# Performance work log

Measured on AMD Instinct MI355X. Metric: run time of the kernel, lower is better.

## Reference

```python
import jax, jax.numpy as jnp
import numpy as np

B, S, D, H, F = 2, 1024, 2048, 16, 8192
DH = D // H
MAX_ALPHA = 0.2
CN_SCALE = D / (D - 1)  # CenterNorm scale factor dim/(dim-1)


def setup_inputs() -> dict:
    key = jax.random.key(0)
    ks = jax.random.split(key, 8)
    s = 0.02
    f32 = jnp.float32
    return {
        "x": jax.random.normal(ks[0], (B, S, D), f32),
        "ln1_g": jnp.ones((D,), f32), "ln1_b": jnp.zeros((D,), f32),
        "wq": jax.random.normal(ks[1], (D, D), f32) * s, "bq": jnp.zeros((D,), f32),
        "wk": jax.random.normal(ks[2], (D, D), f32) * s, "bk": jnp.zeros((D,), f32),
        "wv": jax.random.normal(ks[3], (D, D), f32) * s, "bv": jnp.zeros((D,), f32),
        "wo": jax.random.normal(ks[4], (D, D), f32) * s, "bo": jnp.zeros((D,), f32),
        "tau": jnp.ones((H,), f32),   # learnable per-head temperature, init_tau=1.0
        "nu": jnp.ones((H,), f32),    # learnable per-head output scale, init_nu=1.0
        "alpha1": jnp.full((D,), 0.1, f32),  # per-channel residual weight, init 0.1
        "ln2_g": jnp.ones((D,), f32), "ln2_b": jnp.zeros((D,), f32),
        "w1": jax.random.normal(ks[5], (F, D), f32) * s, "b1": jnp.zeros((F,), f32),
        "w2": jax.random.normal(ks[6], (D, F), f32) * s, "b2": jnp.zeros((D,), f32),
        "alpha2": jnp.full((D,), 0.1, f32),
    }


def _center_norm(x, g, b):
    # CenterNorm: subtract mean only (no variance), scale by dim/(dim-1)
    mu = jnp.mean(x, axis=-1, keepdims=True)
    return g * (CN_SCALE * (x - mu)) + b


def _l2norm(t):
    return t / (jnp.linalg.norm(t, axis=-1, keepdims=True) + 1e-6)


def _cosine_attn(x, wq, bq, wk, bk, wv, bv, wo, bo, tau, nu):
    # project and split heads -> [B,H,S,DH]
    def proj(w, b):
        return (jnp.einsum('bsd,ed->bse', x, w) + b).reshape(B, S, H, DH).transpose(0, 2, 1, 3)
    q, k, v = proj(wq, bq), proj(wk, bk), proj(wv, bv)
    qn, kn = _l2norm(q), _l2norm(k)  # cosine similarity attention
    scores = jnp.einsum('bhqd,bhkd->bhqk', qn, kn) * tau[None, :, None, None]
    causal = jnp.tril(jnp.ones((S, S), bool))
    scores = jnp.where(causal[None, None], scores, -jnp.inf)
    p = jax.nn.softmax(scores, axis=-1)
    o = jnp.einsum('bhqk,bhkd->bhqd', p, v) * nu[None, :, None, None]
    o = o.transpose(0, 2, 1, 3).reshape(B, S, D)
    return jnp.einsum('bsd,ed->bse', o, wo) + bo


def _ffn(x, w1, b1, w2, b2):
    h = jax.nn.gelu(jnp.einsum('bsd,fd->bsf', x, w1) + b1)
    return jnp.einsum('bsf,df->bsd', h, w2) + b2


def reference(x, ln1_g, ln1_b, wq, bq, wk, bk, wv, bv, wo, bo, tau, nu,
              alpha1, ln2_g, ln2_b, w1, b1, w2, b2, alpha2):
    a = _center_norm(x, ln1_g, ln1_b)
    a1 = jnp.clip(alpha1, -MAX_ALPHA, MAX_ALPHA)
    x1 = a + a1 * _cosine_attn(a, wq, bq, wk, bk, wv, bv, wo, bo, tau, nu)
    m = _center_norm(x1, ln2_g, ln2_b)
    a2 = jnp.clip(alpha2, -MAX_ALPHA, MAX_ALPHA)
    return m + a2 * _ffn(m, w1, b1, w2, b2)
```

## Files before the change

### kernel.cpp

```cpp
#include <hip/hip_runtime.h>
#include <hip/hip_bf16.h>
#include <stdint.h>

#define B_ 2
#define S_ 1024
#define D_ 2048
#define H_ 16
#define F_ 8192
#define DH_ 128
#define M_ 2048

typedef unsigned short u16;
typedef __attribute__((ext_vector_type(8))) short short8;
typedef __attribute__((ext_vector_type(4))) float f32x4;
typedef __attribute__((ext_vector_type(2))) float f32x2;

__device__ __forceinline__ u16 f2bf(float f) {
  union { float f; uint32_t u; } c; c.f = f;
  uint32_t r = c.u + 0x7FFFu + ((c.u >> 16) & 1u);
  return (u16)(r >> 16);
}

__device__ __forceinline__ float bf2f(u16 v) {
  union { uint32_t u; float f; } c; c.u = ((uint32_t)v) << 16;
  return c.f;
}

__device__ __forceinline__ void gload16(const void* g, void* l) {
  __builtin_amdgcn_global_load_lds((const __attribute__((address_space(1))) void*)g,
                                   (__attribute__((address_space(3))) void*)l, 16, 0, 0);
}

__device__ __forceinline__ float clipa(float a) {
  return fminf(0.2f, fmaxf(-0.2f, a));
}

__device__ __forceinline__ float gelu_f(float x) {
  float z = 0.7978845608028654f * (x + 0.044715f * x * x * x);
  z = fminf(10.f, fmaxf(-10.f, z));
  float e = __expf(2.f * z);
  return 0.5f * x * (1.f + (e - 1.f) / (e + 1.f));
}

__global__ __launch_bounds__(256) void k_cvt_half(const float* __restrict__ wq,
                                                  const float* __restrict__ wk,
                                                  const float* __restrict__ wv,
                                                  const float* __restrict__ wo,
                                                  const float* __restrict__ w1,
                                                  const float* __restrict__ w2,
                                                  u16* __restrict__ dst, int base) {
  const int gi = base + blockIdx.x * 256 + threadIdx.x;
  const float* s;
  int off;
  if (gi < 2097152) {
    int r = gi >> 19;
    s = r == 0 ? wq : (r == 1 ? wk : (r == 2 ? wv : wo));
    off = gi & 524287;
  } else if (gi < 4194304) {
    s = w1; off = gi - 2097152;
  } else {
    s = w2; off = gi - 4194304;
  }
  f32x4 a = *(const f32x4*)(s + (size_t)off * 8);
  f32x4 b = *(const f32x4*)(s + (size_t)off * 8 + 4);
  short8 o;
  o[0] = (short)f2bf(a[0]); o[1] = (short)f2bf(a[1]);
  o[2] = (short)f2bf(a[2]); o[3] = (short)f2bf(a[3]);
  o[4] = (short)f2bf(b[0]); o[5] = (short)f2bf(b[1]);
  o[6] = (short)f2bf(b[2]); o[7] = (short)f2bf(b[3]);
  *(short8*)(dst + (size_t)gi * 8) = o;
}

__global__ __launch_bounds__(256) void k_centernorm(const float* __restrict__ x,
                                                    const float* __restrict__ g,
                                                    const float* __restrict__ bb,
                                                    float* __restrict__ of,
                                                    u16* __restrict__ ob) {
  const int row = blockIdx.x;
  const int t = threadIdx.x;
  const float* xr = x + (size_t)row * D_;
  f32x4 v0 = *(const f32x4*)(xr + t * 8);
  f32x4 v1 = *(const f32x4*)(xr + t * 8 + 4);
  float s = v0[0] + v0[1] + v0[2] + v0[3] + v1[0] + v1[1] + v1[2] + v1[3];
#pragma unroll
  for (int off = 1; off < 64; off <<= 1) s += __shfl_xor(s, off);
  __shared__ float red[4];
  if ((t & 63) == 0) red[t >> 6] = s;
  __syncthreads();
  const float mu = (red[0] + red[1] + red[2] + red[3]) * (1.0f / D_);
  const float CNS = (float)D_ / (float)(D_ - 1);
  f32x4 g0 = *(const f32x4*)(g + t * 8);
  f32x4 g1 = *(const f32x4*)(g + t * 8 + 4);
  f32x4 b0 = *(const f32x4*)(bb + t * 8);
  f32x4 b1 = *(const f32x4*)(bb + t * 8 + 4);
  f32x4 y0, y1;
  short8 yb;
#pragma unroll
  for (int i = 0; i < 4; i++) {
    y0[i] = g0[i] * (CNS * (v0[i] - mu)) + b0[i];
    y1[i] = g1[i] * (CNS * (v1[i] - mu)) + b1[i];
  }
#pragma unroll
  for (int i = 0; i < 4; i++) { yb[i] = (short)f2bf(y0[i]); yb[4 + i] = (short)f2bf(y1[i]); }
  float* orow = of + (size_t)row * D_;
  *(f32x4*)(orow + t * 8) = y0;
  *(f32x4*)(orow + t * 8 + 4) = y1;
  *(short8*)(ob + (size_t)row * D_ + t * 8) = yb;
}

template <int EPI>
__device__ __forceinline__ void gemm256_core(const u16* __restrict__ A,
                                             const u16* __restrict__ Bt,
                                             const float* __restrict__ bias,
                                             float* __restrict__ outf,
                                             u16* __restrict__ outb,
                                             int N, int K, int kbase, int nk,
                                             int m0, int n0,
                                             const float* __restrict__ tau,
                                             u16* __restrict__ qkv, int z) {
  __shared__ char lds[2][65536];
  const int t = threadIdx.x;
  const int l = t & 63, w = t >> 6;
  const int wr = w >> 2, wc = w & 3;
  const int l15 = l & 15, lhi = l >> 4;
  const int sw = (l15 & 7) << 4;
  const int ab0 = l15 * 128 + ((lhi * 16) ^ sw);
  const int ab1 = l15 * 128 + ((64 + lhi * 16) ^ sw);

  auto stage = [&](int kt, int h) {
#pragma unroll
    for (int rj = 0; rj < 4; rj++) {
      const int region = rj >> 1, j = rj & 1;
      const int pl = h * 16384 + j * 8192 + t * 16;
      const int row = pl >> 7;
      const int scol = (pl & 127) ^ ((row & 7) << 4);
      const int grow = (region ? n0 : m0) + row;
      const char* src = (const char*)(region ? Bt : A) +
                        (size_t)grow * (size_t)(K * 2) +
                        (size_t)((kbase + kt * 64) * 2 + scol);
      gload16(src, &lds[kt & 1][region * 32768 + pl]);
    }
  };

  f32x4 acc[8][4] = {};

  stage(0, 0); stage(0, 1); stage(1, 0);
  asm volatile("s_waitcnt vmcnt(4)" ::: "memory");
  __builtin_amdgcn_s_barrier();
  __builtin_amdgcn_sched_barrier(0);

  for (int kt = 0; kt < nk; ++kt) {
    const char* base = &lds[kt & 1][0];
    const char* pA0 = base + wr * 4096 + ab0;
    const char* pA1 = base + wr * 4096 + ab1;
    const char* pB0 = base + 32768 + wc * 8192 + ab0;
    const char* pB1 = base + 32768 + wc * 8192 + ab1;
    short8 bf[4][2];
#pragma unroll
    for (int ni = 0; ni < 4; ni++) {
      bf[ni][0] = *(const short8*)(pB0 + ni * 2048);
      bf[ni][1] = *(const short8*)(pB1 + ni * 2048);
    }
#pragma unroll
    for (int q = 0; q < 4; q++) {
      short8 aq[2][2];
#pragma unroll
      for (int mi = 0; mi < 2; mi++) {
        aq[mi][0] = *(const short8*)(pA0 + q * 8192 + mi * 2048);
        aq[mi][1] = *(const short8*)(pA1 + q * 8192 + mi * 2048);
      }
      if (q == 1 && kt + 1 < nk) stage(kt + 1, 1);
      if (q == 3 && kt + 2 < nk) stage(kt + 2, 0);
      __builtin_amdgcn_s_setprio(1);
#pragma unroll
      for (int ks = 0; ks < 2; ks++)
#pragma unroll
        for (int mi = 0; mi < 2; mi++)
#pragma unroll
          for (int ni = 0; ni < 4; ni++)
            acc[q * 2 + mi][ni] = __builtin_amdgcn_mfma_f32_16x16x32_bf16(
                aq[mi][ks], bf[ni][ks], acc[q * 2 + mi][ni], 0, 0, 0);
      __builtin_amdgcn_s_setprio(0);
      if (q == 1) __builtin_amdgcn_s_barrier();
    }
    if (kt + 1 < nk) {
      if (kt + 2 < nk) { asm volatile("s_waitcnt vmcnt(4)" ::: "memory"); }
      else             { asm volatile("s_waitcnt vmcnt(0)" ::: "memory"); }
      __builtin_amdgcn_s_barrier();
      __builtin_amdgcn_sched_barrier(0);
    }
  }

  if constexpr (EPI == 4) {
    __shared__ float part[4][256];
#pragma unroll
    for (int ni = 0; ni < 4; ni++) {
      const float bc = bias[n0 + wc * 64 + ni * 16 + l15];
#pragma unroll
      for (int ai = 0; ai < 8; ai++)
#pragma unroll
        for (int j = 0; j < 4; j++) acc[ai][ni][j] += bc;
    }
    if (z < 2) {
      float p[8][4];
#pragma unroll
      for (int ai = 0; ai < 8; ai++)
#pragma unroll
        for (int j = 0; j < 4; j++) {
          p[ai][j] = acc[ai][0][j] * acc[ai][0][j] + acc[ai][1][j] * acc[ai][1][j] +
                     acc[ai][2][j] * acc[ai][2][j] + acc[ai][3][j] * acc[ai][3][j];
#pragma unroll
          for (int off = 1; off < 16; off <<= 1) p[ai][j] += __shfl_xor(p[ai][j], off);
        }
      if (l15 == 0) {
#pragma unroll
        for (int ai = 0; ai < 8; ai++)
#pragma unroll
          for (int j = 0; j < 4; j++) {
            const int rb = (ai >> 1) * 64 + wr * 32 + (ai & 1) * 16 + lhi * 4 + j;
            part[wc][rb] = p[ai][j];
          }
      }
    }
    __syncthreads();
    const int hl = wc >> 1;
    const int hglob = (n0 >> 7) + hl;
    const float tauh = (z == 0) ? tau[hglob] : 1.f;
    char* yt = (char*)&lds[0][0] + w * 16384;
#pragma unroll
    for (int ai = 0; ai < 8; ai++) {
#pragma unroll
      for (int j = 0; j < 4; j++) {
        float sc = 1.f;
        if (z < 2) {
          const int rb = (ai >> 1) * 64 + wr * 32 + (ai & 1) * 16 + lhi * 4 + j;
          const float ssq = part[2 * hl][rb] + part[2 * hl + 1][rb];
          sc = tauh / (sqrtf(ssq) + 1e-6f);
        }
        const int rl = (ai >> 1) * 32 + (ai & 1) * 16 + lhi * 4 + j;
        const int swz = (rl & 7) << 4;
#pragma unroll
        for (int ni = 0; ni < 4; ni++) {
          const int cbyte = (ni * 16 + l15) * 2;
          *(u16*)(yt + rl * 128 + (cbyte ^ swz)) = f2bf(acc[ai][ni][j] * sc);
        }
      }
    }
    __syncthreads();
#pragma unroll
    for (int pass = 0; pass < 16; pass++) {
      const int rl = pass * 8 + (l >> 3);
      const int cb = (l & 7) * 16;
      const short8 v = *(const short8*)(yt + rl * 128 + (cb ^ ((rl & 7) << 4)));
      const int m = m0 + ((rl >> 5) << 6) + wr * 32 + (rl & 31);
      const int bb2 = m >> 10, s = m & 1023;
      const int d = (wc & 1) * 64 + (cb >> 1);
      *(short8*)(qkv + (((size_t)(bb2 * H_ + hglob)) * S_ + s) * DH_ + d) = v;
    }
    return;
  }

#pragma unroll
  for (int ni = 0; ni < 4; ni++) {
    const int col = n0 + wc * 64 + ni * 16 + l15;
    const float bcol = (EPI == 3) ? 0.f : bias[col];
#pragma unroll
    for (int ai = 0; ai < 8; ai++) {
      const int row = m0 + (ai >> 1) * 64 + wr * 32 + (ai & 1) * 16 + lhi * 4;
#pragma unroll
      for (int j = 0; j < 4; j++) {
        const float v = acc[ai][ni][j] + bcol;
        const size_t idx = (size_t)(row + j) * N + col;
        if (EPI == 0) outf[idx] = v;
        else if (EPI == 2) outb[idx] = f2bf(gelu_f(v));
        else outb[idx] = f2bf(v);
      }
    }
  }
}

__global__ __launch_bounds__(512, 2) void k_qkv256(const u16* A, const u16* W,
                                                   const float* b0, const float* b1,
                                                   const float* b2, const float* tau,
                                                   u16* qn, u16* kn, u16* vn) {
  const int z = blockIdx.z;
  const u16* Bt = W + (size_t)z * 4194304;
  const float* bias = z == 0 ? b0 : (z == 1 ? b1 : b2);
  u16* dst = z == 0 ? qn : (z == 1 ? kn : vn);
  gemm256_core<4>(A, Bt, bias, nullptr, nullptr, D_, D_, 0, 32,
                  blockIdx.y * 256, blockIdx.x * 256, tau, dst, z);
}

__global__ __launch_bounds__(512, 2) void k_ffn1_256(const u16* A, const u16* Bt,
                                                     const float* bias, u16* outb) {
  gemm256_core<2>(A, Bt, bias, nullptr, outb, F_, D_, 0, 32,
                  blockIdx.y * 256, blockIdx.x * 256, nullptr, nullptr, 0);
}

__global__ __launch_bounds__(512, 2) void k_ffn2_256(const u16* A, const u16* Bt, u16* P) {
  gemm256_core<3>(A, Bt, nullptr, nullptr, P + (size_t)blockIdx.z * M_ * D_, D_, F_,
                  blockIdx.z * 2048, 32, blockIdx.y * 256, blockIdx.x * 256,
                  nullptr, nullptr, 0);
}

__global__ __launch_bounds__(256, 2) void k_oproj(const u16* __restrict__ A,
                                                  const u16* __restrict__ Bt,
                                                  const float* __restrict__ bias,
                                                  const float* __restrict__ res,
                                                  const float* __restrict__ alpha,
                                                  float* __restrict__ outf) {
  const int N = D_, K = D_, nk = 32;
  const int m0 = blockIdx.y * 128, n0 = blockIdx.x * 128;
  __shared__ char lds[2][32768];
  const int t = threadIdx.x;
  const int l = t & 63, w = t >> 6;
  const int wr = w >> 1, wc = w & 1;
  const int l15 = l & 15, lhi = l >> 4;
  const int sw = (l15 & 7) << 4;
  const int ab0 = l15 * 128 + ((lhi * 16) ^ sw);
  const int ab1 = l15 * 128 + ((64 + lhi * 16) ^ sw);

  auto stage = [&](int kt, int h) {
#pragma unroll
    for (int rj = 0; rj < 4; rj++) {
      const int region = rj >> 1, j = rj & 1;
      const int pl = h * 8192 + j * 4096 + t * 16;
      const int row = pl >> 7;
      const int scol = (pl & 127) ^ ((row & 7) << 4);
      const int grow = (region ? n0 : m0) + row;
      const char* src = (const char*)(region ? Bt : A) +
                        (size_t)grow * (size_t)(K * 2) + (size_t)(kt * 128 + scol);
      gload16(src, &lds[kt & 1][region * 16384 + pl]);
    }
  };

  f32x4 acc[4][4] = {};
  stage(0, 0); stage(0, 1); stage(1, 0);
  asm volatile("s_waitcnt vmcnt(4)" ::: "memory");
  __builtin_amdgcn_s_barrier();
  __builtin_amdgcn_sched_barrier(0);

  for (int kt = 0; kt < nk; ++kt) {
    const char* base = &lds[kt & 1][0];
    const char* pB0 = base + 16384 + wc * 8192 + ab0;
    const char* pB1 = base + 16384 + wc * 8192 + ab1;
    short8 bf[4][2];
#pragma unroll
    for (int ni = 0; ni < 4; ni++) {
      bf[ni][0] = *(const short8*)(pB0 + ni * 2048);
      bf[ni][1] = *(const short8*)(pB1 + ni * 2048);
    }
#pragma unroll
    for (int q = 0; q < 2; q++) {
      short8 aq[2][2];
#pragma unroll
      for (int mi = 0; mi < 2; mi++) {
        aq[mi][0] = *(const short8*)(base + q * 8192 + wr * 4096 + mi * 2048 + ab0);
        aq[mi][1] = *(const short8*)(base + q * 8192 + wr * 4096 + mi * 2048 + ab1);
      }
      if (q == 0 && kt + 1 < nk) stage(kt + 1, 1);
      if (q == 1 && kt + 2 < nk) stage(kt + 2, 0);
      __builtin_amdgcn_s_setprio(1);
#pragma unroll
      for (int ks = 0; ks < 2; ks++)
#pragma unroll
        for (int mi = 0; mi < 2; mi++)
#pragma unroll
          for (int ni = 0; ni < 4; ni++)
            acc[q * 2 + mi][ni] = __builtin_amdgcn_mfma_f32_16x16x32_bf16(
                aq[mi][ks], bf[ni][ks], acc[q * 2 + mi][ni], 0, 0, 0);
      __builtin_amdgcn_s_setprio(0);
      if (q == 0) __builtin_amdgcn_s_barrier();
    }
    if (kt + 1 < nk) {
      if (kt + 2 < nk) { asm volatile("s_waitcnt vmcnt(4)" ::: "memory"); }
      else             { asm volatile("s_waitcnt vmcnt(0)" ::: "memory"); }
      __builtin_amdgcn_s_barrier();
      __builtin_amdgcn_sched_barrier(0);
    }
  }

#pragma unroll
  for (int ni = 0; ni < 4; ni++) {
    const int col = n0 + wc * 64 + ni * 16 + l15;
    const float bcol = bias[col];
    const float alc = clipa(alpha[col]);
#pragma unroll
    for (int ai = 0; ai < 4; ai++) {
      const int row = m0 + (ai >> 1) * 64 + wr * 32 + (ai & 1) * 16 + lhi * 4;
#pragma unroll
      for (int j = 0; j < 4; j++) {
        const size_t idx = (size_t)(row + j) * N + col;
        outf[idx] = res[idx] + alc * (acc[ai][ni][j] + bcol);
      }
    }
  }
}

__global__ __launch_bounds__(256) void k_ffn2_combine(const u16* __restrict__ P,
                                                      const float* __restrict__ bias,
                                                      const float* __restrict__ res,
                                                      const float* __restrict__ alpha,
                                                      float* __restrict__ out) {
  const int i = blockIdx.x * 256 + threadIdx.x;
  const size_t base = (size_t)i * 8;
  const int col = (int)(base & (D_ - 1));
  const size_t PS = (size_t)M_ * D_;
  float s[8] = {};
#pragma unroll
  for (int p = 0; p < 4; p++) {
    short8 v = *(const short8*)(P + p * PS + base);
#pragma unroll
    for (int j = 0; j < 8; j++) s[j] += bf2f((u16)v[j]);
  }
  f32x4 b0 = *(const f32x4*)(bias + col);
  f32x4 b1 = *(const f32x4*)(bias + col + 4);
  f32x4 a0 = *(const f32x4*)(alpha + col);
  f32x4 a1 = *(const f32x4*)(alpha + col + 4);
  f32x4 r0 = *(const f32x4*)(res + base);
  f32x4 r1 = *(const f32x4*)(res + base + 4);
  f32x4 o0, o1;
#pragma unroll
  for (int j = 0; j < 4; j++) {
    o0[j] = r0[j] + clipa(a0[j]) * (s[j] + b0[j]);
    o1[j] = r1[j] + clipa(a1[j]) * (s[4 + j] + b1[j]);
  }
  *(f32x4*)(out + base) = o0;
  *(f32x4*)(out + base + 4) = o1;
}

__global__ __launch_bounds__(256) void k_attn(const u16* __restrict__ qn,
                                              const u16* __restrict__ kn,
                                              const u16* __restrict__ vn,
                                              const float* __restrict__ nu,
                                              u16* __restrict__ o) {
  __shared__ u16 Ks[64 * 128];
  __shared__ u16 Vt[128 * 64];
  __shared__ u16 Pl[4][16][72];
  const int t = threadIdx.x;
  const int l = t & 63, w = t >> 6;
  const int l15 = l & 15, lhi = l >> 4;
  const int qt = blockIdx.x;
  const int bh = blockIdx.y;
  const int h = bh & (H_ - 1);
  const int b = bh >> 4;
  const size_t hoff = (size_t)bh * S_ * DH_;
  const u16* Qh = qn + hoff;
  const u16* Kh = kn + hoff;
  const u16* Vh = vn + hoff;
  const int q0 = qt * 64;
  const int r0 = q0 + w * 16;
  short8 qf[4];
#pragma unroll
  for (int kk = 0; kk < 4; kk++)
    qf[kk] = *(const short8*)(Qh + (size_t)(r0 + l15) * DH_ + kk * 32 + lhi * 8);
  float mrow[4], lrow[4];
  f32x4 oacc[8] = {};
#pragma unroll
  for (int j = 0; j < 4; j++) { mrow[j] = -1e30f; lrow[j] = 0.f; }

  for (int kv0 = 0; kv0 < q0 + 64; kv0 += 64) {
#pragma unroll
    for (int i = 0; i < 4; i++) {
      const int p = i * 4096 + t * 16;
      const int row = p >> 8;
      const int colb = p & 255;
      const int scolb = colb ^ ((row & 7) << 4);
      gload16((const char*)(Kh + (size_t)(kv0 + row) * DH_) + scolb, (char*)Ks + p);
    }
#pragma unroll
    for (int i = 0; i < 4; i++) {
      const int c0 = w * 8 + i * 32;
      const int r = l;
      short8 vv = *(const short8*)(Vh + (size_t)(kv0 + r) * DH_ + c0);
#pragma unroll
      for (int j = 0; j < 8; j++) {
        const int ba = ((c0 + j) * 128 + r * 2) ^ (((c0 + j) & 7) << 4);
        *(u16*)((char*)Vt + ba) = (u16)vv[j];
      }
    }
    __syncthreads();
    f32x4 st[4] = {};
#pragma unroll
    for (int ks = 0; ks < 4; ks++) {
#pragma unroll
      for (int ct = 0; ct < 4; ct++) {
        const int n = ct * 16 + l15;
        const int ka = (ks * 32 + lhi * 8) * 2;
        short8 kf = *(const short8*)((const char*)Ks + n * 256 + (ka ^ ((n & 7) << 4)));
        st[ct] = __builtin_amdgcn_mfma_f32_16x16x32_bf16(qf[ks], kf, st[ct], 0, 0, 0);
      }
    }
    float pm[4] = {-1e30f, -1e30f, -1e30f, -1e30f};
#pragma unroll
    for (int ct = 0; ct < 4; ct++) {
      const int col = kv0 + ct * 16 + l15;
#pragma unroll
      for (int j = 0; j < 4; j++) {
        const int row = r0 + lhi * 4 + j;
        float s = st[ct][j];
        s = (col <= row) ? s : -1e30f;
        st[ct][j] = s;
        pm[j] = fmaxf(pm[j], s);
      }
    }
#pragma unroll
    for (int j = 0; j < 4; j++) {
#pragma unroll
      for (int off = 1; off < 16; off <<= 1) pm[j] = fmaxf(pm[j], __shfl_xor(pm[j], off));
    }
    float scl[4], psum[4];
#pragma unroll
    for (int j = 0; j < 4; j++) {
      const float nm = fmaxf(mrow[j], pm[j]);
      scl[j] = __expf(mrow[j] - nm);
      mrow[j] = nm;
      psum[j] = 0.f;
    }
#pragma unroll
    for (int ct = 0; ct < 4; ct++) {
#pragma unroll
      for (int j = 0; j < 4; j++) {
        const float p = __expf(st[ct][j] - mrow[j]);
        psum[j] += p;
        Pl[w][lhi * 4 + j][ct * 16 + l15] = f2bf(p);
      }
    }
#pragma unroll
    for (int j = 0; j < 4; j++) {
#pragma unroll
      for (int off = 1; off < 16; off <<= 1) psum[j] += __shfl_xor(psum[j], off);
      lrow[j] = lrow[j] * scl[j] + psum[j];
    }
#pragma unroll
    for (int nt = 0; nt < 8; nt++) {
#pragma unroll
      for (int j = 0; j < 4; j++) oacc[nt][j] *= scl[j];
    }
#pragma unroll
    for (int ks2 = 0; ks2 < 2; ks2++) {
      short8 pa = *(const short8*)((const char*)&Pl[w][0][0] + l15 * 144 + ks2 * 64 + lhi * 16);
#pragma unroll
      for (int nt = 0; nt < 8; nt++) {
        const int n = nt * 16 + l15;
        const int ba = (n * 128 + (ks2 * 32 + lhi * 8) * 2) ^ ((n & 7) << 4);
        short8 vf = *(const short8*)((const char*)Vt + ba);
        oacc[nt] = __builtin_amdgcn_mfma_f32_16x16x32_bf16(pa, vf, oacc[nt], 0, 0, 0);
      }
    }
    __syncthreads();
  }
  const float num = nu[h];
  float rs[4];
#pragma unroll
  for (int j = 0; j < 4; j++) rs[j] = num / lrow[j];
#pragma unroll
  for (int nt = 0; nt < 8; nt++) {
    const int col = h * DH_ + nt * 16 + l15;
#pragma unroll
    for (int j = 0; j < 4; j++) {
      const int row = r0 + lhi * 4 + j;
      o[((size_t)b * S_ + row) * D_ + col] = f2bf(oacc[nt][j] * rs[j]);
    }
  }
}

extern "C" void kernel_launch(void* const* d_in, const int* in_sizes, int n_in,
                              void* d_out, int out_size, void* d_ws, size_t ws_size,
                              hipStream_t stream) {
  const float* x    = (const float*)d_in[0];
  const float* ln1g = (const float*)d_in[1];
  const float* ln1b = (const float*)d_in[2];
  const float* wq   = (const float*)d_in[3];
  const float* bq   = (const float*)d_in[4];
  const float* wk   = (const float*)d_in[5];
  const float* bk   = (const float*)d_in[6];
  const float* wv   = (const float*)d_in[7];
  const float* bv   = (const float*)d_in[8];
  const float* wo   = (const float*)d_in[9];
  const float* bo   = (const float*)d_in[10];
  const float* tau  = (const float*)d_in[11];
  const float* nu   = (const float*)d_in[12];
  const float* al1  = (const float*)d_in[13];
  const float* ln2g = (const float*)d_in[14];
  const float* ln2b = (const float*)d_in[15];
  const float* w1   = (const float*)d_in[16];
  const float* b1   = (const float*)d_in[17];
  const float* w2   = (const float*)d_in[18];
  const float* b2   = (const float*)d_in[19];
  const float* al2  = (const float*)d_in[20];

  char* ws = (char*)d_ws;
  u16* WQ = (u16*)(ws + 0);
  u16* WO = (u16*)(ws + 25165824);
  u16* W1B = (u16*)(ws + 33554432);
  u16* W2B = (u16*)(ws + 67108864);
  float* AF = (float*)(ws + 100663296);
  u16*   AB = (u16*)(ws + 117440512);
  u16*   OB = (u16*)(ws + 125829120);
  u16*   MB = (u16*)(ws + 134217728);
  float* X1 = (float*)(ws + 142606336);
  float* MF2 = (float*)(ws + 159383552);
  u16* QN = (u16*)(ws + 176160768);
  u16* KN = (u16*)(ws + 184549376);
  u16* VN = (u16*)(ws + 192937984);
  u16*   HB = (u16*)(ws + 176160768);
  u16*   P4 = (u16*)(ws + 0);

  k_cvt_half<<<12288, 256, 0, stream>>>(wq, wk, wv, wo, w1, w2, WQ, 0);
  k_cvt_half<<<12288, 256, 0, stream>>>(wq, wk, wv, wo, w1, w2, WQ, 3145728);

  k_centernorm<<<M_, 256, 0, stream>>>(x, ln1g, ln1b, AF, AB);

  k_qkv256<<<dim3(8, 8, 3), 512, 0, stream>>>(AB, WQ, bq, bk, bv, tau, QN, KN, VN);

  k_attn<<<dim3(S_ / 64, B_ * H_), 256, 0, stream>>>(QN, KN, VN, nu, OB);

  k_oproj<<<dim3(16, 16), 256, 0, stream>>>(OB, WO, bo, AF, al1, X1);

  k_centernorm<<<M_, 256, 0, stream>>>(X1, ln2g, ln2b, MF2, MB);

  k_ffn1_256<<<dim3(32, 8), 512, 0, stream>>>(MB, W1B, b1, HB);

  k_ffn2_256<<<dim3(8, 8, 4), 512, 0, stream>>>(HB, W2B, P4);
  k_ffn2_combine<<<2048, 256, 0, stream>>>(P4, b2, MF2, al2, (float*)d_out);
}
```

Baseline: 372.5 us.

## Merge weight conversion into one kernel and rework GEMM staging pipeline

The two weight-conversion launches are replaced by one kernel in which each thread converts four 8-element chunks, with all loads issued before any conversion to raise memory-level parallelism. The 256-tile GEMM core now splits the next-tile global-to-LDS loads into four quarter-stages, one per inner q step, so B and A for the next k-tile are fetched in pieces across the compute of the current tile. Extra barriers and lgkmcnt waits are added every quarter step. That spreads memory traffic more evenly but adds synchronisation and reduces prefetch depth from two tiles to one.

```diff
diff --git a/kernel.cpp b/kernel.cpp
--- a/kernel.cpp
+++ b/kernel.cpp
@@ -42,33 +42,49 @@
   return 0.5f * x * (1.f + (e - 1.f) / (e + 1.f));
 }
 
-__global__ __launch_bounds__(256) void k_cvt_half(const float* __restrict__ wq,
-                                                  const float* __restrict__ wk,
-                                                  const float* __restrict__ wv,
-                                                  const float* __restrict__ wo,
-                                                  const float* __restrict__ w1,
-                                                  const float* __restrict__ w2,
-                                                  u16* __restrict__ dst, int base) {
-  const int gi = base + blockIdx.x * 256 + threadIdx.x;
-  const float* s;
-  int off;
-  if (gi < 2097152) {
-    int r = gi >> 19;
-    s = r == 0 ? wq : (r == 1 ? wk : (r == 2 ? wv : wo));
-    off = gi & 524287;
-  } else if (gi < 4194304) {
-    s = w1; off = gi - 2097152;
-  } else {
-    s = w2; off = gi - 4194304;
-  }
-  f32x4 a = *(const f32x4*)(s + (size_t)off * 8);
-  f32x4 b = *(const f32x4*)(s + (size_t)off * 8 + 4);
-  short8 o;
-  o[0] = (short)f2bf(a[0]); o[1] = (short)f2bf(a[1]);
-  o[2] = (short)f2bf(a[2]); o[3] = (short)f2bf(a[3]);
-  o[4] = (short)f2bf(b[0]); o[5] = (short)f2bf(b[1]);
-  o[6] = (short)f2bf(b[2]); o[7] = (short)f2bf(b[3]);
-  *(short8*)(dst + (size_t)gi * 8) = o;
+__global__ __launch_bounds__(256) void k_cvt_all(const float* __restrict__ wq,
+                                                 const float* __restrict__ wk,
+                                                 const float* __restrict__ wv,
+                                                 const float* __restrict__ wo,
+                                                 const float* __restrict__ w1,
+                                                 const float* __restrict__ w2,
+                                                 u16* __restrict__ dst) {
+  const int tid = blockIdx.x * 256 + threadIdx.x;
+  const float* s[4];
+  int gi[4];
+#pragma unroll
+  for (int k = 0; k < 4; k++) {
+    const int g = tid + k * 1572864;
+    gi[k] = g;
+    const float* p;
+    int off;
+    if (g < 2097152) {
+      const int r = g >> 19;
+      p = r == 0 ? wq : (r == 1 ? wk : (r == 2 ? wv : wo));
+      off = g & 524287;
+    } else if (g < 4194304) {
+      p = w1; off = g - 2097152;
+    } else {
+      p = w2; off = g - 4194304;
+    }
+    s[k] = p + (size_t)off * 8;
+  }
+  f32x4 a[4], b[4];
+#pragma unroll
+  for (int k = 0; k < 4; k++) {
+    a[k] = *(const f32x4*)(s[k]);
+    b[k] = *(const f32x4*)(s[k] + 4);
+  }
+  __builtin_amdgcn_sched_barrier(0);
+#pragma unroll
+  for (int k = 0; k < 4; k++) {
+    short8 o;
+    o[0] = (short)f2bf(a[k][0]); o[1] = (short)f2bf(a[k][1]);
+    o[2] = (short)f2bf(a[k][2]); o[3] = (short)f2bf(a[k][3]);
+    o[4] = (short)f2bf(b[k][0]); o[5] = (short)f2bf(b[k][1]);
+    o[6] = (short)f2bf(b[k][2]); o[7] = (short)f2bf(b[k][3]);
+    *(short8*)(dst + (size_t)gi[k] * 8) = o;
+  }
 }
 
 __global__ __launch_bounds__(256) void k_centernorm(const float* __restrict__ x,
@@ -127,25 +143,26 @@
   const int ab0 = l15 * 128 + ((lhi * 16) ^ sw);
   const int ab1 = l15 * 128 + ((64 + lhi * 16) ^ sw);
 
-  auto stage = [&](int kt, int h) {
-#pragma unroll
-    for (int rj = 0; rj < 4; rj++) {
-      const int region = rj >> 1, j = rj & 1;
+  auto stageu = [&](int kt, int u) {
+    const int reg = (u < 2) ? 1 : 0;
+    const int h = u & 1;
+#pragma unroll
+    for (int j = 0; j < 2; j++) {
       const int pl = h * 16384 + j * 8192 + t * 16;
       const int row = pl >> 7;
       const int scol = (pl & 127) ^ ((row & 7) << 4);
-      const int grow = (region ? n0 : m0) + row;
-      const char* src = (const char*)(region ? Bt : A) +
+      const int grow = (reg ? n0 : m0) + row;
+      const char* src = (const char*)(reg ? Bt : A) +
                         (size_t)grow * (size_t)(K * 2) +
                         (size_t)((kbase + kt * 64) * 2 + scol);
-      gload16(src, &lds[kt & 1][region * 32768 + pl]);
+      gload16(src, &lds[kt & 1][reg * 32768 + pl]);
     }
   };
 
   f32x4 acc[8][4] = {};
 
-  stage(0, 0); stage(0, 1); stage(1, 0);
-  asm volatile("s_waitcnt vmcnt(4)" ::: "memory");
+  stageu(0, 0); stageu(0, 1); stageu(0, 2); stageu(0, 3);
+  asm volatile("s_waitcnt vmcnt(2)" ::: "memory");
   __builtin_amdgcn_s_barrier();
   __builtin_amdgcn_sched_barrier(0);
 
@@ -155,22 +172,27 @@
     const char* pA1 = base + wr * 4096 + ab1;
     const char* pB0 = base + 32768 + wc * 8192 + ab0;
     const char* pB1 = base + 32768 + wc * 8192 + ab1;
+    const bool more = (kt + 1 < nk);
     short8 bf[4][2];
 #pragma unroll
-    for (int ni = 0; ni < 4; ni++) {
-      bf[ni][0] = *(const short8*)(pB0 + ni * 2048);
-      bf[ni][1] = *(const short8*)(pB1 + ni * 2048);
-    }
-#pragma unroll
     for (int q = 0; q < 4; q++) {
+      if (q == 0) {
+#pragma unroll
+        for (int ni = 0; ni < 4; ni++) {
+          bf[ni][0] = *(const short8*)(pB0 + ni * 2048);
+          bf[ni][1] = *(const short8*)(pB1 + ni * 2048);
+        }
+      }
       short8 aq[2][2];
 #pragma unroll
       for (int mi = 0; mi < 2; mi++) {
         aq[mi][0] = *(const short8*)(pA0 + q * 8192 + mi * 2048);
         aq[mi][1] = *(const short8*)(pA1 + q * 8192 + mi * 2048);
       }
-      if (q == 1 && kt + 1 < nk) stage(kt + 1, 1);
-      if (q == 3 && kt + 2 < nk) stage(kt + 2, 0);
+      if (more) stageu(kt + 1, q);
+      __builtin_amdgcn_s_barrier();
+      asm volatile("s_waitcnt lgkmcnt(0)" ::: "memory");
+      __builtin_amdgcn_sched_barrier(0);
       __builtin_amdgcn_s_setprio(1);
 #pragma unroll
       for (int ks = 0; ks < 2; ks++)
@@ -181,13 +203,20 @@
             acc[q * 2 + mi][ni] = __builtin_amdgcn_mfma_f32_16x16x32_bf16(
                 aq[mi][ks], bf[ni][ks], acc[q * 2 + mi][ni], 0, 0, 0);
       __builtin_amdgcn_s_setprio(0);
-      if (q == 1) __builtin_amdgcn_s_barrier();
-    }
-    if (kt + 1 < nk) {
-      if (kt + 2 < nk) { asm volatile("s_waitcnt vmcnt(4)" ::: "memory"); }
-      else             { asm volatile("s_waitcnt vmcnt(0)" ::: "memory"); }
-      __builtin_amdgcn_s_barrier();
-      __builtin_amdgcn_sched_barrier(0);
+      if (q == 1) {
+        if (more) { asm volatile("s_waitcnt vmcnt(4)" ::: "memory"); }
+        else      { asm volatile("s_waitcnt vmcnt(0)" ::: "memory"); }
+        __builtin_amdgcn_s_barrier();
+        __builtin_amdgcn_sched_barrier(0);
+      } else if (q == 3) {
+        if (more) {
+          asm volatile("s_waitcnt vmcnt(2)" ::: "memory");
+          __builtin_amdgcn_s_barrier();
+          __builtin_amdgcn_sched_barrier(0);
+        }
+      } else {
+        __builtin_amdgcn_s_barrier();
+      }
     }
   }
 
@@ -607,8 +636,7 @@
   u16*   HB = (u16*)(ws + 176160768);
   u16*   P4 = (u16*)(ws + 0);
 
-  k_cvt_half<<<12288, 256, 0, stream>>>(wq, wk, wv, wo, w1, w2, WQ, 0);
-  k_cvt_half<<<12288, 256, 0, stream>>>(wq, wk, wv, wo, w1, w2, WQ, 3145728);
+  k_cvt_all<<<6144, 256, 0, stream>>>(wq, wk, wv, wo, w1, w2, WQ);
 
   k_centernorm<<<M_, 256, 0, stream>>>(x, ln1g, ln1b, AF, AB);
 
```

Result: no change. 378.8 us (+1.7%).

## Add lockstep-pipelined 256-tile GEMM core for FFN kernels

Applied to the files above, without the earlier changes.

Adds a separate 256x256 GEMM core for the two FFN GEMMs. It issues the next K-tile's global-to-LDS loads in four quarter-chunks, one interleaved with each MFMA quarter, and places waitcnt/barrier points at quarter boundaries instead of one wait per K-step. The goal is to spread memory traffic across the compute phase so loads and MFMAs overlap better. The original core is specialised to the QKV epilogue only, and unused output parameters are removed. The finer barrier scheme adds more sync points and is harder to keep race-free.

```diff
diff --git a/kernel.cpp b/kernel.cpp
--- a/kernel.cpp
+++ b/kernel.cpp
@@ -112,8 +112,6 @@
 __device__ __forceinline__ void gemm256_core(const u16* __restrict__ A,
                                              const u16* __restrict__ Bt,
                                              const float* __restrict__ bias,
-                                             float* __restrict__ outf,
-                                             u16* __restrict__ outb,
                                              int N, int K, int kbase, int nk,
                                              int m0, int n0,
                                              const float* __restrict__ tau,
@@ -191,73 +189,164 @@
     }
   }
 
-  if constexpr (EPI == 4) {
-    __shared__ float part[4][256];
-#pragma unroll
-    for (int ni = 0; ni < 4; ni++) {
-      const float bc = bias[n0 + wc * 64 + ni * 16 + l15];
+  __shared__ float part[4][256];
+#pragma unroll
+  for (int ni = 0; ni < 4; ni++) {
+    const float bc = bias[n0 + wc * 64 + ni * 16 + l15];
+#pragma unroll
+    for (int ai = 0; ai < 8; ai++)
+#pragma unroll
+      for (int j = 0; j < 4; j++) acc[ai][ni][j] += bc;
+  }
+  if (z < 2) {
+    float p[8][4];
+#pragma unroll
+    for (int ai = 0; ai < 8; ai++)
+#pragma unroll
+      for (int j = 0; j < 4; j++) {
+        p[ai][j] = acc[ai][0][j] * acc[ai][0][j] + acc[ai][1][j] * acc[ai][1][j] +
+                   acc[ai][2][j] * acc[ai][2][j] + acc[ai][3][j] * acc[ai][3][j];
+#pragma unroll
+        for (int off = 1; off < 16; off <<= 1) p[ai][j] += __shfl_xor(p[ai][j], off);
+      }
+    if (l15 == 0) {
 #pragma unroll
       for (int ai = 0; ai < 8; ai++)
 #pragma unroll
-        for (int j = 0; j < 4; j++) acc[ai][ni][j] += bc;
-    }
-    if (z < 2) {
-      float p[8][4];
-#pragma unroll
-      for (int ai = 0; ai < 8; ai++)
-#pragma unroll
         for (int j = 0; j < 4; j++) {
-          p[ai][j] = acc[ai][0][j] * acc[ai][0][j] + acc[ai][1][j] * acc[ai][1][j] +
-                     acc[ai][2][j] * acc[ai][2][j] + acc[ai][3][j] * acc[ai][3][j];
-#pragma unroll
-          for (int off = 1; off < 16; off <<= 1) p[ai][j] += __shfl_xor(p[ai][j], off);
+          const int rb = (ai >> 1) * 64 + wr * 32 + (ai & 1) * 16 + lhi * 4 + j;
+          part[wc][rb] = p[ai][j];
         }
-      if (l15 == 0) {
-#pragma unroll
-        for (int ai = 0; ai < 8; ai++)
-#pragma unroll
-          for (int j = 0; j < 4; j++) {
-            const int rb = (ai >> 1) * 64 + wr * 32 + (ai & 1) * 16 + lhi * 4 + j;
-            part[wc][rb] = p[ai][j];
-          }
-      }
-    }
-    __syncthreads();
-    const int hl = wc >> 1;
-    const int hglob = (n0 >> 7) + hl;
-    const float tauh = (z == 0) ? tau[hglob] : 1.f;
-    char* yt = (char*)&lds[0][0] + w * 16384;
-#pragma unroll
-    for (int ai = 0; ai < 8; ai++) {
-#pragma unroll
-      for (int j = 0; j < 4; j++) {
-        float sc = 1.f;
-        if (z < 2) {
-          const int rb = (ai >> 1) * 64 + wr * 32 + (ai & 1) * 16 + lhi * 4 + j;
-          const float ssq = part[2 * hl][rb] + part[2 * hl + 1][rb];
-          sc = tauh / (sqrtf(ssq) + 1e-6f);
+    }
+  }
+  __syncthreads();
+  const int hl = wc >> 1;
+  const int hglob = (n0 >> 7) + hl;
+  const float tauh = (z == 0) ? tau[hglob] : 1.f;
+  char* yt = (char*)&lds[0][0] + w * 16384;
+#pragma unroll
+  for (int ai = 0; ai < 8; ai++) {
+#pragma unroll
+    for (int j = 0; j < 4; j++) {
+      float sc = 1.f;
+      if (z < 2) {
+        const int rb = (ai >> 1) * 64 + wr * 32 + (ai & 1) * 16 + lhi * 4 + j;
+        const float ssq = part[2 * hl][rb] + part[2 * hl + 1][rb];
+        sc = tauh / (sqrtf(ssq) + 1e-6f);
+      }
+      const int rl = (ai >> 1) * 32 + (ai & 1) * 16 + lhi * 4 + j;
+      const int swz = (rl & 7) << 4;
+#pragma unroll
+      for (int ni = 0; ni < 4; ni++) {
+        const int cbyte = (ni * 16 + l15) * 2;
+        *(u16*)(yt + rl * 128 + (cbyte ^ swz)) = f2bf(acc[ai][ni][j] * sc);
+      }
+    }
+  }
+  __syncthreads();
+#pragma unroll
+  for (int pass = 0; pass < 16; pass++) {
+    const int rl = pass * 8 + (l >> 3);
+    const int cb = (l & 7) * 16;
+    const short8 v = *(const short8*)(yt + rl * 128 + (cb ^ ((rl & 7) << 4)));
+    const int m = m0 + ((rl >> 5) << 6) + wr * 32 + (rl & 31);
+    const int bb2 = m >> 10, s = m & 1023;
+    const int d = (wc & 1) * 64 + (cb >> 1);
+    *(short8*)(qkv + (((size_t)(bb2 * H_ + hglob)) * S_ + s) * DH_ + d) = v;
+  }
+}
+
+template <int EPI>
+__device__ __forceinline__ void gemm256_lock(const u16* __restrict__ A,
+                                             const u16* __restrict__ Bt,
+                                             const float* __restrict__ bias,
+                                             u16* __restrict__ outb,
+                                             int N, int K, int kbase, int nk,
+                                             int m0, int n0) {
+  __shared__ char lds[2][65536];
+  const int t = threadIdx.x;
+  const int l = t & 63, w = t >> 6;
+  const int wr = w >> 2, wc = w & 3;
+  const int l15 = l & 15, lhi = l >> 4;
+  const int sw = (l15 & 7) << 4;
+  const int ab0 = l15 * 128 + ((lhi * 16) ^ sw);
+  const int ab1 = l15 * 128 + ((64 + lhi * 16) ^ sw);
+
+  auto stageu = [&](int kt, int u) {
+    const int reg = (u < 2) ? 1 : 0;
+    const int h = u & 1;
+#pragma unroll
+    for (int j = 0; j < 2; j++) {
+      const int pl = h * 16384 + j * 8192 + t * 16;
+      const int row = pl >> 7;
+      const int scol = (pl & 127) ^ ((row & 7) << 4);
+      const int grow = (reg ? n0 : m0) + row;
+      const char* src = (const char*)(reg ? Bt : A) +
+                        (size_t)grow * (size_t)(K * 2) +
+                        (size_t)((kbase + kt * 64) * 2 + scol);
+      gload16(src, &lds[kt & 1][reg * 32768 + pl]);
+    }
+  };
+
+  f32x4 acc[8][4] = {};
+
+  stageu(0, 0); stageu(0, 1); stageu(0, 2); stageu(0, 3);
+  asm volatile("s_waitcnt vmcnt(2)" ::: "memory");
+  __builtin_amdgcn_s_barrier();
+  __builtin_amdgcn_sched_barrier(0);
+
+  for (int kt = 0; kt < nk; ++kt) {
+    const char* base = &lds[kt & 1][0];
+    const char* pA0 = base + wr * 4096 + ab0;
+    const char* pA1 = base + wr * 4096 + ab1;
+    const char* pB0 = base + 32768 + wc * 8192 + ab0;
+    const char* pB1 = base + 32768 + wc * 8192 + ab1;
+    const bool more = (kt + 1 < nk);
+    short8 bf[4][2];
+#pragma unroll
+    for (int q = 0; q < 4; q++) {
+      if (q == 0) {
+#pragma unroll
+        for (int ni = 0; ni < 4; ni++) {
+          bf[ni][0] = *(const short8*)(pB0 + ni * 2048);
+          bf[ni][1] = *(const short8*)(pB1 + ni * 2048);
         }
-        const int rl = (ai >> 1) * 32 + (ai & 1) * 16 + lhi * 4 + j;
-        const int swz = (rl & 7) << 4;
-#pragma unroll
-        for (int ni = 0; ni < 4; ni++) {
-          const int cbyte = (ni * 16 + l15) * 2;
-          *(u16*)(yt + rl * 128 + (cbyte ^ swz)) = f2bf(acc[ai][ni][j] * sc);
+      }
+      short8 aq[2][2];
+#pragma unroll
+      for (int mi = 0; mi < 2; mi++) {
+        aq[mi][0] = *(const short8*)(pA0 + q * 8192 + mi * 2048);
+        aq[mi][1] = *(const short8*)(pA1 + q * 8192 + mi * 2048);
+      }
+      if (more) stageu(kt + 1, q);
+      __builtin_amdgcn_s_barrier();
+      asm volatile("s_waitcnt lgkmcnt(0)" ::: "memory");
+      __builtin_amdgcn_sched_barrier(0);
+      __builtin_amdgcn_s_setprio(1);
+#pragma unroll
+      for (int ks = 0; ks < 2; ks++)
+#pragma unroll
+        for (int mi = 0; mi < 2; mi++)
+#pragma unroll
+          for (int ni = 0; ni < 4; ni++)
+            acc[q * 2 + mi][ni] = __builtin_amdgcn_mfma_f32_16x16x32_bf16(
+                aq[mi][ks], bf[ni][ks], acc[q * 2 + mi][ni], 0, 0, 0);
+      __builtin_amdgcn_s_setprio(0);
+      if (q == 1) {
+        if (more) { asm volatile("s_waitcnt vmcnt(4)" ::: "memory"); }
+        else      { asm volatile("s_waitcnt vmcnt(0)" ::: "memory"); }
+        __builtin_amdgcn_s_barrier();
+        __builtin_amdgcn_sched_barrier(0);
+      } else if (q == 3) {
+        if (more) {
+          asm volatile("s_waitcnt vmcnt(2)" ::: "memory");
+          __builtin_amdgcn_s_barrier();
+          __builtin_amdgcn_sched_barrier(0);
         }
-      }
-    }
-    __syncthreads();
-#pragma unroll
-    for (int pass = 0; pass < 16; pass++) {
-      const int rl = pass * 8 + (l >> 3);
-      const int cb = (l & 7) * 16;
-      const short8 v = *(const short8*)(yt + rl * 128 + (cb ^ ((rl & 7) << 4)));
-      const int m = m0 + ((rl >> 5) << 6) + wr * 32 + (rl & 31);
-      const int bb2 = m >> 10, s = m & 1023;
-      const int d = (wc & 1) * 64 + (cb >> 1);
-      *(short8*)(qkv + (((size_t)(bb2 * H_ + hglob)) * S_ + s) * DH_ + d) = v;
-    }
-    return;
+      } else {
+        __builtin_amdgcn_s_barrier();
+      }
+    }
   }
 
 #pragma unroll
@@ -271,8 +360,7 @@
       for (int j = 0; j < 4; j++) {
         const float v = acc[ai][ni][j] + bcol;
         const size_t idx = (size_t)(row + j) * N + col;
-        if (EPI == 0) outf[idx] = v;
-        else if (EPI == 2) outb[idx] = f2bf(gelu_f(v));
+        if (EPI == 2) outb[idx] = f2bf(gelu_f(v));
         else outb[idx] = f2bf(v);
       }
     }
@@ -287,20 +375,19 @@
   const u16* Bt = W + (size_t)z * 4194304;
   const float* bias = z == 0 ? b0 : (z == 1 ? b1 : b2);
   u16* dst = z == 0 ? qn : (z == 1 ? kn : vn);
-  gemm256_core<4>(A, Bt, bias, nullptr, nullptr, D_, D_, 0, 32,
+  gemm256_core<4>(A, Bt, bias, D_, D_, 0, 32,
                   blockIdx.y * 256, blockIdx.x * 256, tau, dst, z);
 }
 
 __global__ __launch_bounds__(512, 2) void k_ffn1_256(const u16* A, const u16* Bt,
                                                      const float* bias, u16* outb) {
-  gemm256_core<2>(A, Bt, bias, nullptr, outb, F_, D_, 0, 32,
-                  blockIdx.y * 256, blockIdx.x * 256, nullptr, nullptr, 0);
+  gemm256_lock<2>(A, Bt, bias, outb, F_, D_, 0, 32,
+                  blockIdx.y * 256, blockIdx.x * 256);
 }
 
 __global__ __launch_bounds__(512, 2) void k_ffn2_256(const u16* A, const u16* Bt, u16* P) {
-  gemm256_core<3>(A, Bt, nullptr, nullptr, P + (size_t)blockIdx.z * M_ * D_, D_, F_,
-                  blockIdx.z * 2048, 32, blockIdx.y * 256, blockIdx.x * 256,
-                  nullptr, nullptr, 0);
+  gemm256_lock<3>(A, Bt, nullptr, P + (size_t)blockIdx.z * M_ * D_, D_, F_,
+                  blockIdx.z * 2048, 32, blockIdx.y * 256, blockIdx.x * 256);
 }
 
 __global__ __launch_bounds__(256, 2) void k_oproj(const u16* __restrict__ A,
```

After: 369.7 us. Within noise of the previous version (-0.8%).

## Fuse weight conversion into centernorm and attention kernels to overlap work

Applied to the files above, without the earlier changes.

Removes the standalone weight-conversion launches. The q/k/v/o weight cast is appended as extra blocks to the first CenterNorm kernel, and the w1/w2 cast is appended as extra blocks to the attention kernel using a flattened grid. The aim is to hide memory-bound conversion behind the causal attention's imbalanced tail and to save launches. The risk is bandwidth contention with attention and a different block scheduling order.

```diff
diff --git a/kernel.cpp b/kernel.cpp
--- a/kernel.cpp
+++ b/kernel.cpp
@@ -42,40 +42,31 @@
   return 0.5f * x * (1.f + (e - 1.f) / (e + 1.f));
 }
 
-__global__ __launch_bounds__(256) void k_cvt_half(const float* __restrict__ wq,
-                                                  const float* __restrict__ wk,
-                                                  const float* __restrict__ wv,
-                                                  const float* __restrict__ wo,
-                                                  const float* __restrict__ w1,
-                                                  const float* __restrict__ w2,
-                                                  u16* __restrict__ dst, int base) {
-  const int gi = base + blockIdx.x * 256 + threadIdx.x;
-  const float* s;
-  int off;
-  if (gi < 2097152) {
-    int r = gi >> 19;
-    s = r == 0 ? wq : (r == 1 ? wk : (r == 2 ? wv : wo));
-    off = gi & 524287;
-  } else if (gi < 4194304) {
-    s = w1; off = gi - 2097152;
-  } else {
-    s = w2; off = gi - 4194304;
-  }
-  f32x4 a = *(const f32x4*)(s + (size_t)off * 8);
-  f32x4 b = *(const f32x4*)(s + (size_t)off * 8 + 4);
-  short8 o;
-  o[0] = (short)f2bf(a[0]); o[1] = (short)f2bf(a[1]);
-  o[2] = (short)f2bf(a[2]); o[3] = (short)f2bf(a[3]);
-  o[4] = (short)f2bf(b[0]); o[5] = (short)f2bf(b[1]);
-  o[6] = (short)f2bf(b[2]); o[7] = (short)f2bf(b[3]);
-  *(short8*)(dst + (size_t)gi * 8) = o;
-}
-
-__global__ __launch_bounds__(256) void k_centernorm(const float* __restrict__ x,
-                                                    const float* __restrict__ g,
-                                                    const float* __restrict__ bb,
-                                                    float* __restrict__ of,
-                                                    u16* __restrict__ ob) {
+__global__ __launch_bounds__(256) void k_cn1_cvt(const float* __restrict__ x,
+                                                 const float* __restrict__ g,
+                                                 const float* __restrict__ bb,
+                                                 float* __restrict__ of,
+                                                 u16* __restrict__ ob,
+                                                 const float* __restrict__ wq,
+                                                 const float* __restrict__ wk,
+                                                 const float* __restrict__ wv,
+                                                 const float* __restrict__ wo,
+                                                 u16* __restrict__ dstW) {
+  if (blockIdx.x >= 2048) {
+    const int gi = (blockIdx.x - 2048) * 256 + threadIdx.x;
+    const int r = gi >> 19;
+    const float* s = r == 0 ? wq : (r == 1 ? wk : (r == 2 ? wv : wo));
+    const int off = gi & 524287;
+    f32x4 a = *(const f32x4*)(s + (size_t)off * 8);
+    f32x4 b = *(const f32x4*)(s + (size_t)off * 8 + 4);
+    short8 o;
+    o[0] = (short)f2bf(a[0]); o[1] = (short)f2bf(a[1]);
+    o[2] = (short)f2bf(a[2]); o[3] = (short)f2bf(a[3]);
+    o[4] = (short)f2bf(b[0]); o[5] = (short)f2bf(b[1]);
+    o[6] = (short)f2bf(b[2]); o[7] = (short)f2bf(b[3]);
+    *(short8*)(dstW + (size_t)gi * 8) = o;
+    return;
+  }
   const int row = blockIdx.x;
   const int t = threadIdx.x;
   const float* xr = x + (size_t)row * D_;
@@ -108,11 +99,47 @@
   *(short8*)(ob + (size_t)row * D_ + t * 8) = yb;
 }
 
+__global__ __launch_bounds__(256) void k_centernorm(const float* __restrict__ x,
+                                                    const float* __restrict__ g,
+                                                    const float* __restrict__ bb,
+                                                    float* __restrict__ of,
+                                                    u16* __restrict__ ob) {
+  const int row = blockIdx.x;
+  const int t = threadIdx.x;
+  const float* xr = x + (size_t)row * D_;
+  f32x4 v0 = *(const f32x4*)(xr + t * 8);
+  f32x4 v1 = *(const f32x4*)(xr + t * 8 + 4);
+  float s = v0[0] + v0[1] + v0[2] + v0[3] + v1[0] + v1[1] + v1[2] + v1[3];
+#pragma unroll
+  for (int off = 1; off < 64; off <<= 1) s += __shfl_xor(s, off);
+  __shared__ float red[4];
+  if ((t & 63) == 0) red[t >> 6] = s;
+  __syncthreads();
+  const float mu = (red[0] + red[1] + red[2] + red[3]) * (1.0f / D_);
+  const float CNS = (float)D_ / (float)(D_ - 1);
+  f32x4 g0 = *(const f32x4*)(g + t * 8);
+  f32x4 g1 = *(const f32x4*)(g + t * 8 + 4);
+  f32x4 b0 = *(const f32x4*)(bb + t * 8);
+  f32x4 b1 = *(const f32x4*)(bb + t * 8 + 4);
+  f32x4 y0, y1;
+  short8 yb;
+#pragma unroll
+  for (int i = 0; i < 4; i++) {
+    y0[i] = g0[i] * (CNS * (v0[i] - mu)) + b0[i];
+    y1[i] = g1[i] * (CNS * (v1[i] - mu)) + b1[i];
+  }
+#pragma unroll
+  for (int i = 0; i < 4; i++) { yb[i] = (short)f2bf(y0[i]); yb[4 + i] = (short)f2bf(y1[i]); }
+  float* orow = of + (size_t)row * D_;
+  *(f32x4*)(orow + t * 8) = y0;
+  *(f32x4*)(orow + t * 8 + 4) = y1;
+  *(short8*)(ob + (size_t)row * D_ + t * 8) = yb;
+}
+
 template <int EPI>
 __device__ __forceinline__ void gemm256_core(const u16* __restrict__ A,
                                              const u16* __restrict__ Bt,
                                              const float* __restrict__ bias,
-                                             float* __restrict__ outf,
                                              u16* __restrict__ outb,
                                              int N, int K, int kbase, int nk,
                                              int m0, int n0,
@@ -271,8 +298,7 @@
       for (int j = 0; j < 4; j++) {
         const float v = acc[ai][ni][j] + bcol;
         const size_t idx = (size_t)(row + j) * N + col;
-        if (EPI == 0) outf[idx] = v;
-        else if (EPI == 2) outb[idx] = f2bf(gelu_f(v));
+        if (EPI == 2) outb[idx] = f2bf(gelu_f(v));
         else outb[idx] = f2bf(v);
       }
     }
@@ -287,18 +313,18 @@
   const u16* Bt = W + (size_t)z * 4194304;
   const float* bias = z == 0 ? b0 : (z == 1 ? b1 : b2);
   u16* dst = z == 0 ? qn : (z == 1 ? kn : vn);
-  gemm256_core<4>(A, Bt, bias, nullptr, nullptr, D_, D_, 0, 32,
+  gemm256_core<4>(A, Bt, bias, nullptr, D_, D_, 0, 32,
                   blockIdx.y * 256, blockIdx.x * 256, tau, dst, z);
 }
 
 __global__ __launch_bounds__(512, 2) void k_ffn1_256(const u16* A, const u16* Bt,
                                                      const float* bias, u16* outb) {
-  gemm256_core<2>(A, Bt, bias, nullptr, outb, F_, D_, 0, 32,
+  gemm256_core<2>(A, Bt, bias, outb, F_, D_, 0, 32,
                   blockIdx.y * 256, blockIdx.x * 256, nullptr, nullptr, 0);
 }
 
 __global__ __launch_bounds__(512, 2) void k_ffn2_256(const u16* A, const u16* Bt, u16* P) {
-  gemm256_core<3>(A, Bt, nullptr, nullptr, P + (size_t)blockIdx.z * M_ * D_, D_, F_,
+  gemm256_core<3>(A, Bt, nullptr, P + (size_t)blockIdx.z * M_ * D_, D_, F_,
                   blockIdx.z * 2048, 32, blockIdx.y * 256, blockIdx.x * 256,
                   nullptr, nullptr, 0);
 }
@@ -433,15 +459,32 @@
                                               const u16* __restrict__ kn,
                                               const u16* __restrict__ vn,
                                               const float* __restrict__ nu,
-                                              u16* __restrict__ o) {
+                                              u16* __restrict__ o,
+                                              const float* __restrict__ w1,
+                                              const float* __restrict__ w2,
+                                              u16* __restrict__ W12) {
   __shared__ u16 Ks[64 * 128];
   __shared__ u16 Vt[128 * 64];
   __shared__ u16 Pl[4][16][72];
+  if (blockIdx.x >= 512) {
+    const int gi = (blockIdx.x - 512) * 256 + threadIdx.x;
+    const float* s = (gi < 2097152) ? w1 : w2;
+    const int off = (gi < 2097152) ? gi : gi - 2097152;
+    f32x4 a = *(const f32x4*)(s + (size_t)off * 8);
+    f32x4 b = *(const f32x4*)(s + (size_t)off * 8 + 4);
+    short8 ov;
+    ov[0] = (short)f2bf(a[0]); ov[1] = (short)f2bf(a[1]);
+    ov[2] = (short)f2bf(a[2]); ov[3] = (short)f2bf(a[3]);
+    ov[4] = (short)f2bf(b[0]); ov[5] = (short)f2bf(b[1]);
+    ov[6] = (short)f2bf(b[2]); ov[7] = (short)f2bf(b[3]);
+    *(short8*)(W12 + (size_t)gi * 8) = ov;
+    return;
+  }
   const int t = threadIdx.x;
   const int l = t & 63, w = t >> 6;
   const int l15 = l & 15, lhi = l >> 4;
-  const int qt = blockIdx.x;
-  const int bh = blockIdx.y;
+  const int qt = blockIdx.x & 15;
+  const int bh = blockIdx.x >> 4;
   const int h = bh & (H_ - 1);
   const int b = bh >> 4;
   const size_t hoff = (size_t)bh * S_ * DH_;
@@ -594,7 +637,6 @@
   u16* WQ = (u16*)(ws + 0);
   u16* WO = (u16*)(ws + 25165824);
   u16* W1B = (u16*)(ws + 33554432);
-  u16* W2B = (u16*)(ws + 67108864);
   float* AF = (float*)(ws + 100663296);
   u16*   AB = (u16*)(ws + 117440512);
   u16*   OB = (u16*)(ws + 125829120);
@@ -606,15 +648,13 @@
   u16* VN = (u16*)(ws + 192937984);
   u16*   HB = (u16*)(ws + 176160768);
   u16*   P4 = (u16*)(ws + 0);
-
-  k_cvt_half<<<12288, 256, 0, stream>>>(wq, wk, wv, wo, w1, w2, WQ, 0);
-  k_cvt_half<<<12288, 256, 0, stream>>>(wq, wk, wv, wo, w1, w2, WQ, 3145728);
-
-  k_centernorm<<<M_, 256, 0, stream>>>(x, ln1g, ln1b, AF, AB);
+  u16* W2B = (u16*)(ws + 67108864);
+
+  k_cn1_cvt<<<10240, 256, 0, stream>>>(x, ln1g, ln1b, AF, AB, wq, wk, wv, wo, WQ);
 
   k_qkv256<<<dim3(8, 8, 3), 512, 0, stream>>>(AB, WQ, bq, bk, bv, tau, QN, KN, VN);
 
-  k_attn<<<dim3(S_ / 64, B_ * H_), 256, 0, stream>>>(QN, KN, VN, nu, OB);
+  k_attn<<<16896, 256, 0, stream>>>(QN, KN, VN, nu, OB, w1, w2, W1B);
 
   k_oproj<<<dim3(16, 16), 256, 0, stream>>>(OB, WO, bo, AF, al1, X1);
 
```

After: 369.9 us. About the same (-0.7%).
